# Kernel tuning notes

Measured on AMD Instinct MI355X. Metric: run time of the kernel, lower is better.

The kernel has to match this reference:

```python
import jax, jax.numpy as jnp
import numpy as np

B, N, SEQ, PRED = 32, 128, 336, 96
DIN, DEMB, HID, G, K = 16, 32, 64, 8, 25
END = DEMB + 2  # 2 decomposition channels + dy embedding
T = SEQ + PRED


def setup_inputs() -> dict:
    key = jax.random.key(0)
    ks = jax.random.split(key, 22)
    s = 0.02
    p = lambda k, shape: jax.random.normal(k, shape, dtype=jnp.float32) * s
    return {
        "x": jax.random.normal(ks[0], (B, N, SEQ), dtype=jnp.float32),
        "dy": jax.random.normal(ks[1], (B, N, T, DIN), dtype=jnp.float32),
        "gi": jax.random.randint(ks[2], (N,), 0, G),
        "dy_w": p(ks[3], (DEMB, DIN)), "dy_b": p(ks[4], (DEMB,)),
        "w_seas": p(ks[5], (G, PRED, SEQ)), "b_seas": p(ks[6], (G, PRED)),
        "w_trend": p(ks[7], (G, PRED, SEQ)), "b_trend": p(ks[8], (G, PRED)),
        "w_res": p(ks[9], (G, PRED, SEQ)), "b_res": p(ks[10], (G, PRED)),
        "w1_end": p(ks[11], (G, HID, END)), "b1_end": p(ks[12], (G, HID)),
        "w2_end": p(ks[13], (G, 1, HID)), "b2_end": p(ks[14], (G, 1)),
        "w_ih": p(ks[15], (3 * HID, END)), "w_hh": p(ks[16], (3 * HID, HID)),
        "b_ih": p(ks[17], (3 * HID,)), "b_hh": p(ks[18], (3 * HID,)),
        "w_ap": p(ks[19], (1, HID)), "b_ap": p(ks[20], (1,)),
    }


def _moving_avg(x, k):
    # x: [b, seq, n]; edge-padded moving average over time (Autoformer series_decomp)
    pad = (k - 1) // 2
    xp = jnp.pad(x, ((0, 0), (pad, pad), (0, 0)), mode="edge")
    cs = jnp.cumsum(xp, axis=1)
    cs = jnp.concatenate([jnp.zeros_like(cs[:, :1]), cs], axis=1)
    return (cs[:, k:] - cs[:, :-k]) / k


def _gru(xseq, w_ih, w_hh, b_ih, b_hh):
    # torch nn.GRU, batch_first, gate order (r, z, n)
    h0 = jnp.zeros((xseq.shape[0], w_hh.shape[1]), dtype=xseq.dtype)
    gx = jnp.einsum("bti,gi->btg", xseq, w_ih) + b_ih  # input-side gates, precomputed
    def step(h, gxt):
        gh = h @ w_hh.T + b_hh
        ir, iz, inn = jnp.split(gxt, 3, axis=-1)
        hr, hz, hn = jnp.split(gh, 3, axis=-1)
        r = jax.nn.sigmoid(ir + hr)
        z = jax.nn.sigmoid(iz + hz)
        ng = jnp.tanh(inn + r * hn)
        h = (1.0 - z) * ng + z * h
        return h, h
    _, ys = jax.lax.scan(step, h0, gx.transpose(1, 0, 2))
    return ys.transpose(1, 0, 2)  # [b, t, hid]


def reference(x, dy, gi, dy_w, dy_b, w_seas, b_seas, w_trend, b_trend,
              w_res, b_res, w1_end, b1_end, w2_end, b2_end,
              w_ih, w_hh, b_ih, b_hh, w_ap, b_ap):
    # global residual path: per-group mean over member nodes
    cnt = jax.ops.segment_sum(jnp.ones((N,), x.dtype), gi, num_segments=G)  # [G]
    gsum = jax.ops.segment_sum(x.transpose(1, 0, 2), gi, num_segments=G)  # [G,b,seq]
    g_in = gsum / cnt[:, None, None]
    g_out = jnp.einsum("gps,gbs->gbp", w_res, g_in) + b_res[:, None, :]

    # series decomposition (node independent -> done once for all nodes)
    xt = x.transpose(0, 2, 1)  # [b, seq, n]
    trend = _moving_avg(xt, K)
    seasonal = xt - trend
    seasonal_init = seasonal.transpose(0, 2, 1)  # [b, n, seq]
    trend_init = trend.transpose(0, 2, 1)

    # per-group Linear(seq->pred) heads, gathered per node (MoE-style dispatch)
    seas_out = jnp.einsum("bns,nps->bnp", seasonal_init, w_seas[gi]) + b_seas[gi][None]
    trend_out = jnp.einsum("bns,nps->bnp", trend_init, w_trend[gi]) + b_trend[gi][None]

    dy_emb = jax.nn.relu(jnp.einsum("bnti,ei->bnte", dy, dy_w) + dy_b)  # [b,n,T,DEMB]

    hidden_former = jnp.concatenate(
        [seasonal_init[..., None], trend_init[..., None], dy_emb[:, :, :SEQ]], axis=-1)
    hidden_after = jnp.concatenate(
        [seas_out[..., None], trend_out[..., None], dy_emb[:, :, SEQ:]], axis=-1)

    # per-group end MLP (Linear -> ReLU -> Linear), weights gathered per node
    w1g, b1g = w1_end[gi], b1_end[gi]
    w2g, b2g = w2_end[gi, 0], b2_end[gi, 0]
    def end_mlp(h):
        z = jax.nn.relu(jnp.einsum("bnte,nhe->bnth", h, w1g) + b1g[None, :, None, :])
        return jnp.einsum("bnth,nh->bnt", z, w2g) + b2g[None, :, None]

    out_former = end_mlp(hidden_former) + g_in[gi].transpose(1, 0, 2)
    out_after = end_mlp(hidden_after) + g_out[gi].transpose(1, 0, 2)

    att_f = _gru(hidden_former.mean(axis=1), w_ih, w_hh, b_ih, b_hh)
    att_a = _gru(hidden_after.mean(axis=1), w_ih, w_hh, b_ih, b_hh)
    atten_former = jax.nn.sigmoid(att_f @ w_ap.T + b_ap)[..., 0]
    atten_after = jax.nn.sigmoid(att_a @ w_ap.T + b_ap)[..., 0]
    return (out_former, atten_former, out_after, atten_after)
```

## Files before the change

### kernel.cpp

```cpp
#include <hip/hip_runtime.h>
#include <math.h>

#define BB 32
#define NN 128
#define SEQL 336
#define PREDL 96
#define DINC 16
#define DEMBC 32
#define HIDC 64
#define GG 8
#define KWIN 25
#define ENDC 34
#define TT 432

#define OFF_SEAS   0
#define OFF_TREND  (OFF_SEAS + BB*NN*SEQL)
#define OFF_GIN    (OFF_TREND + BB*NN*SEQL)
#define OFF_GOUT   (OFF_GIN + GG*BB*SEQL)
#define OFF_SEASO  (OFF_GOUT + GG*BB*PREDL)
#define OFF_TRENDO (OFF_SEASO + BB*NN*PREDL)
#define OFF_GX     (OFF_TRENDO + BB*NN*PREDL)
#define OFF_HIST   (OFF_GX + BB*TT*192)

#define OUT_FORMER 0
#define OUT_ATTF   (BB*NN*SEQL)
#define OUT_AFTER  (OUT_ATTF + BB*SEQL)
#define OUT_ATTA   (OUT_AFTER + BB*NN*PREDL)

__device__ __forceinline__ float fsig(float x) { return 1.0f/(1.0f + __expf(-x)); }
__device__ __forceinline__ float ftanh(float x) { return 1.0f - 2.0f/(__expf(2.0f*x) + 1.0f); }

__global__ __launch_bounds__(384) void k_group_mean(const float* __restrict__ x,
                                                    const int* __restrict__ gi,
                                                    float* __restrict__ g_in) {
    int g = blockIdx.x, b = blockIdx.y;
    __shared__ int sgi[NN];
    __shared__ float scnt;
    int tid = threadIdx.x;
    if (tid < NN) sgi[tid] = gi[tid];
    __syncthreads();
    if (tid == 0) {
        int c = 0;
        for (int n = 0; n < NN; n++) if (sgi[n] == g) c++;
        scnt = (float)c;
    }
    __syncthreads();
    float inv = 1.0f / scnt;
    for (int s = tid; s < SEQL; s += 384) {
        float sum = 0.0f;
        for (int n = 0; n < NN; n++)
            if (sgi[n] == g) sum += x[(b*NN + n)*SEQL + s];
        g_in[(g*BB + b)*SEQL + s] = sum * inv;
    }
}

__global__ void k_gout(const float* __restrict__ g_in, const float* __restrict__ w_res,
                       const float* __restrict__ b_res, float* __restrict__ g_out) {
    int idx = blockIdx.x*blockDim.x + threadIdx.x;
    if (idx >= GG*BB*PREDL) return;
    int p = idx % PREDL;
    int b = (idx / PREDL) % BB;
    int g = idx / (PREDL*BB);
    const float* gr = g_in + (g*BB + b)*SEQL;
    const float* wr = w_res + (g*PREDL + p)*SEQL;
    float acc = b_res[g*PREDL + p];
    for (int s = 0; s < SEQL; s++) acc += gr[s]*wr[s];
    g_out[idx] = acc;
}

__global__ void k_decomp(const float* __restrict__ x, float* __restrict__ seasonal,
                         float* __restrict__ trend) {
    int idx = blockIdx.x*blockDim.x + threadIdx.x;
    if (idx >= BB*NN*SEQL) return;
    int t = idx % SEQL;
    int bn = idx / SEQL;
    const float* xr = x + bn*SEQL;
    float s = 0.0f;
    #pragma unroll
    for (int d = -12; d <= 12; d++) {
        int j = t + d;
        j = j < 0 ? 0 : (j >= SEQL ? SEQL-1 : j);
        s += xr[j];
    }
    float tr = s * (1.0f/KWIN);
    trend[idx] = tr;
    seasonal[idx] = xr[t] - tr;
}

__global__ __launch_bounds__(128) void k_heads(const float* __restrict__ seasonal,
                                               const float* __restrict__ trend,
                                               const int* __restrict__ gi,
                                               const float* __restrict__ w_seas,
                                               const float* __restrict__ b_seas,
                                               const float* __restrict__ w_trend,
                                               const float* __restrict__ b_trend,
                                               float* __restrict__ seas_out,
                                               float* __restrict__ trend_out) {
    int bn = blockIdx.x;
    int n = bn % NN;
    int g = gi[n];
    __shared__ float ss[SEQL];
    __shared__ float st[SEQL];
    for (int s = threadIdx.x; s < SEQL/4; s += 128) {
        ((float4*)ss)[s] = ((const float4*)(seasonal + bn*SEQL))[s];
        ((float4*)st)[s] = ((const float4*)(trend + bn*SEQL))[s];
    }
    __syncthreads();
    int p = threadIdx.x;
    if (p < PREDL) {
        const float4* wsr = (const float4*)(w_seas + (g*PREDL + p)*SEQL);
        const float4* wtr = (const float4*)(w_trend + (g*PREDL + p)*SEQL);
        float a = b_seas[g*PREDL + p];
        float c = b_trend[g*PREDL + p];
        #pragma unroll 4
        for (int s4 = 0; s4 < SEQL/4; s4++) {
            float4 w0 = wsr[s4], w1 = wtr[s4];
            float4 d0 = ((const float4*)ss)[s4], d1 = ((const float4*)st)[s4];
            a += w0.x*d0.x + w0.y*d0.y + w0.z*d0.z + w0.w*d0.w;
            c += w1.x*d1.x + w1.y*d1.y + w1.z*d1.z + w1.w*d1.w;
        }
        seas_out[bn*PREDL + p] = a;
        trend_out[bn*PREDL + p] = c;
    }
}

__global__ __launch_bounds__(64) void k_hmean_gx(
    const float* __restrict__ seasonal, const float* __restrict__ trend,
    const float* __restrict__ seas_out, const float* __restrict__ trend_out,
    const float* __restrict__ dy, const float* __restrict__ dy_w,
    const float* __restrict__ dy_b, const float* __restrict__ w_ih,
    const float* __restrict__ b_ih, const float* __restrict__ b_hh,
    float* __restrict__ gx)
{
    int bt = blockIdx.x;
    int b = bt / TT, t = bt % TT;
    int lane = threadIdx.x;
    float v[ENDC];
    #pragma unroll
    for (int e = 0; e < ENDC; e++) v[e] = 0.0f;
    #pragma unroll
    for (int q = 0; q < 2; q++) {
        int n = lane + q*64;
        int bn = b*NN + n;
        if (t < SEQL) {
            v[0] += seasonal[bn*SEQL + t];
            v[1] += trend[bn*SEQL + t];
        } else {
            int p = t - SEQL;
            v[0] += seas_out[bn*PREDL + p];
            v[1] += trend_out[bn*PREDL + p];
        }
        const float4* dyr = (const float4*)(dy + ((size_t)bn*TT + t)*DINC);
        float4 d0 = dyr[0], d1 = dyr[1], d2 = dyr[2], d3 = dyr[3];
        float dv[DINC] = {d0.x,d0.y,d0.z,d0.w, d1.x,d1.y,d1.z,d1.w,
                          d2.x,d2.y,d2.z,d2.w, d3.x,d3.y,d3.z,d3.w};
        #pragma unroll 4
        for (int e = 0; e < DEMBC; e++) {
            float a = dy_b[e];
            #pragma unroll
            for (int i = 0; i < DINC; i++) a = fmaf(dv[i], dy_w[e*DINC + i], a);
            v[2+e] += fmaxf(a, 0.0f);
        }
    }
    #pragma unroll
    for (int e = 0; e < ENDC; e++) {
        float s = v[e];
        s += __shfl_xor(s, 32, 64);
        s += __shfl_xor(s, 16, 64);
        s += __shfl_xor(s, 8, 64);
        s += __shfl_xor(s, 4, 64);
        s += __shfl_xor(s, 2, 64);
        s += __shfl_xor(s, 1, 64);
        v[e] = s * (1.0f/NN);
    }
    #pragma unroll
    for (int gate = 0; gate < 3; gate++) {
        int j = gate*64 + lane;
        const float* w = w_ih + j*ENDC;
        float a = b_ih[j] + (gate < 2 ? b_hh[j] : 0.0f);
        #pragma unroll
        for (int e = 0; e < ENDC; e++) a = fmaf(v[e], w[e], a);
        gx[(size_t)bt*192 + j] = a;
    }
}

__global__ __launch_bounds__(512, 2) void k_mlp_gru(
    const float* __restrict__ seasonal, const float* __restrict__ trend,
    const float* __restrict__ seas_out, const float* __restrict__ trend_out,
    const float* __restrict__ g_in, const float* __restrict__ g_out,
    const int* __restrict__ gi, const float* __restrict__ dy,
    const float* __restrict__ dy_w, const float* __restrict__ dy_b,
    const float* __restrict__ w1_end, const float* __restrict__ b1_end,
    const float* __restrict__ w2_end, const float* __restrict__ b2_end,
    const float* __restrict__ gx, const float* __restrict__ w_hh,
    const float* __restrict__ b_hh, const float* __restrict__ w_ap,
    const float* __restrict__ b_ap, float* __restrict__ hist,
    float* __restrict__ out)
{
    __shared__ float hs[2*HIDC];
    int tid = threadIdx.x;

    if (blockIdx.x < 64) {
        if (tid >= 64) return;
        int lane = tid;
        int blk = blockIdx.x;
        int b = blk & 31;
        bool former = (blk < 32);
        int steps = former ? SEQL : PREDL;
        int t0 = former ? 0 : SEQL;
        float* hb = hist + (former ? (size_t)b*SEQL*HIDC
                                   : (size_t)BB*SEQL*HIDC + (size_t)b*PREDL*HIDC);
        float wr_[HIDC], wz_[HIDC], wn_[HIDC];
        #pragma unroll
        for (int k = 0; k < HIDC; k++) wr_[k] = w_hh[lane*HIDC + k];
        #pragma unroll
        for (int k = 0; k < HIDC; k++) wz_[k] = w_hh[(lane+64)*HIDC + k];
        #pragma unroll
        for (int k = 0; k < HIDC; k++) wn_[k] = w_hh[(lane+128)*HIDC + k];
        float bhn = b_hh[lane + 128];
        hs[lane] = 0.0f;
        float h = 0.0f;
        const float* gxb = gx + (size_t)(b*TT + t0)*192;
        float c_r = gxb[lane], c_z = gxb[64+lane], c_n = gxb[128+lane];
        float n_r = 0.f, n_z = 0.f, n_n = 0.f;
        if (steps > 1) { n_r = gxb[192+lane]; n_z = gxb[256+lane]; n_n = gxb[320+lane]; }
        for (int s = 0; s < steps; s++) {
            float p_r = 0.f, p_z = 0.f, p_n = 0.f;
            if (s + 2 < steps) {
                const float* gp = gxb + (size_t)(s+2)*192;
                p_r = gp[lane]; p_z = gp[64+lane]; p_n = gp[128+lane];
            }
            const float* hh = hs + (s & 1)*HIDC;
            float ar = 0.f, az = 0.f, an = 0.f;
            #pragma unroll
            for (int k = 0; k < HIDC; k += 4) {
                float4 h4 = *(const float4*)&hh[k];
                ar = fmaf(h4.x, wr_[k],   ar); az = fmaf(h4.x, wz_[k],   az); an = fmaf(h4.x, wn_[k],   an);
                ar = fmaf(h4.y, wr_[k+1], ar); az = fmaf(h4.y, wz_[k+1], az); an = fmaf(h4.y, wn_[k+1], an);
                ar = fmaf(h4.z, wr_[k+2], ar); az = fmaf(h4.z, wz_[k+2], az); an = fmaf(h4.z, wn_[k+2], an);
                ar = fmaf(h4.w, wr_[k+3], ar); az = fmaf(h4.w, wz_[k+3], az); an = fmaf(h4.w, wn_[k+3], an);
            }
            float r = fsig(c_r + ar);
            float z = fsig(c_z + az);
            float tg = ftanh(c_n + r*(bhn + an));
            h = (1.0f - z)*tg + z*h;
            hs[((s+1) & 1)*HIDC + lane] = h;
            hb[(size_t)s*HIDC + lane] = h;
            c_r = n_r; c_z = n_z; c_n = n_n;
            n_r = p_r; n_z = p_z; n_n = p_n;
        }
        float bap = b_ap[0];
        float* attn = out + (former ? (OUT_ATTF + b*SEQL) : (OUT_ATTA + b*PREDL));
        for (int t = lane; t < steps; t += 64) {
            const float* hr = hb + (size_t)t*HIDC;
            float a = 0.f;
            #pragma unroll 16
            for (int k = 0; k < HIDC; k++) a = fmaf(hr[k], w_ap[k], a);
            attn[t] = fsig(a + bap);
        }
        return;
    }

    int bn = blockIdx.x - 64;
    int b = bn / NN, n = bn % NN;
    int g = gi[n];
    int t = tid;
    if (t >= TT) return;

    const float4* dyr = (const float4*)(dy + ((size_t)bn*TT + t)*DINC);
    float4 d0 = dyr[0], d1 = dyr[1], d2 = dyr[2], d3 = dyr[3];
    float dv[DINC] = {d0.x,d0.y,d0.z,d0.w, d1.x,d1.y,d1.z,d1.w,
                      d2.x,d2.y,d2.z,d2.w, d3.x,d3.y,d3.z,d3.w};
    float hv[36];
    #pragma unroll 4
    for (int e = 0; e < DEMBC; e++) {
        float a = dy_b[e];
        #pragma unroll
        for (int i = 0; i < DINC; i++) a = fmaf(dv[i], dy_w[e*DINC + i], a);
        hv[2+e] = fmaxf(a, 0.0f);
    }
    float addv;
    if (t < SEQL) {
        hv[0] = seasonal[bn*SEQL + t];
        hv[1] = trend[bn*SEQL + t];
        addv = g_in[(g*BB + b)*SEQL + t];
    } else {
        int p = t - SEQL;
        hv[0] = seas_out[bn*PREDL + p];
        hv[1] = trend_out[bn*PREDL + p];
        addv = g_out[(g*BB + b)*PREDL + p];
    }
    float acc = b2_end[g];
    const float* w1g = w1_end + g*HIDC*ENDC;
    const float* b1g = b1_end + g*HIDC;
    const float* w2g = w2_end + g*HIDC;
    #pragma unroll 4
    for (int hq = 0; hq < HIDC; hq++) {
        const float* wrow = w1g + hq*ENDC;
        float a = b1g[hq];
        #pragma unroll
        for (int e = 0; e < ENDC; e++) a = fmaf(hv[e], wrow[e], a);
        acc = fmaf(fmaxf(a, 0.0f), w2g[hq], acc);
    }
    acc += addv;
    if (t < SEQL) out[OUT_FORMER + bn*SEQL + t] = acc;
    else          out[OUT_AFTER + bn*PREDL + (t - SEQL)] = acc;
}

extern "C" void kernel_launch(void* const* d_in, const int* in_sizes, int n_in,
                              void* d_out, int out_size, void* d_ws, size_t ws_size,
                              hipStream_t stream) {
    (void)in_sizes; (void)n_in; (void)out_size; (void)ws_size;
    const float* x       = (const float*)d_in[0];
    const float* dy      = (const float*)d_in[1];
    const int*   gi      = (const int*)  d_in[2];
    const float* dy_w    = (const float*)d_in[3];
    const float* dy_b    = (const float*)d_in[4];
    const float* w_seas  = (const float*)d_in[5];
    const float* b_seas  = (const float*)d_in[6];
    const float* w_trend = (const float*)d_in[7];
    const float* b_trend = (const float*)d_in[8];
    const float* w_res   = (const float*)d_in[9];
    const float* b_res   = (const float*)d_in[10];
    const float* w1_end  = (const float*)d_in[11];
    const float* b1_end  = (const float*)d_in[12];
    const float* w2_end  = (const float*)d_in[13];
    const float* b2_end  = (const float*)d_in[14];
    const float* w_ih    = (const float*)d_in[15];
    const float* w_hh    = (const float*)d_in[16];
    const float* b_ih    = (const float*)d_in[17];
    const float* b_hh    = (const float*)d_in[18];
    const float* w_ap    = (const float*)d_in[19];
    const float* b_ap    = (const float*)d_in[20];
    float* ws  = (float*)d_ws;
    float* out = (float*)d_out;

    hipLaunchKernelGGL(k_group_mean, dim3(GG, BB), dim3(384), 0, stream, x, gi, ws + OFF_GIN);
    hipLaunchKernelGGL(k_decomp, dim3((BB*NN*SEQL + 255)/256), dim3(256), 0, stream,
                       x, ws + OFF_SEAS, ws + OFF_TREND);
    hipLaunchKernelGGL(k_gout, dim3((GG*BB*PREDL + 255)/256), dim3(256), 0, stream,
                       ws + OFF_GIN, w_res, b_res, ws + OFF_GOUT);
    hipLaunchKernelGGL(k_heads, dim3(BB*NN), dim3(128), 0, stream,
                       ws + OFF_SEAS, ws + OFF_TREND, gi, w_seas, b_seas, w_trend, b_trend,
                       ws + OFF_SEASO, ws + OFF_TRENDO);
    hipLaunchKernelGGL(k_hmean_gx, dim3(BB*TT), dim3(64), 0, stream,
                       ws + OFF_SEAS, ws + OFF_TREND, ws + OFF_SEASO, ws + OFF_TRENDO,
                       dy, dy_w, dy_b, w_ih, b_ih, b_hh, ws + OFF_GX);
    hipLaunchKernelGGL(k_mlp_gru, dim3(64 + BB*NN), dim3(512), 0, stream,
                       ws + OFF_SEAS, ws + OFF_TREND, ws + OFF_SEASO, ws + OFF_TRENDO,
                       ws + OFF_GIN, ws + OFF_GOUT, gi, dy, dy_w, dy_b,
                       w1_end, b1_end, w2_end, b2_end,
                       ws + OFF_GX, w_hh, b_hh, w_ap, b_ap, ws + OFF_HIST, out);
}
```

Measured before the change: 848.8 us.

## Fuse dy-mean gate projection into end-MLP kernel and split GRU out

Merges the group-mean and residual-head kernels into one, with the group mean kept in shared memory for the head's dot products. The separate per-(b,t) mean and input-gate kernel is folded into a tiled end-MLP kernel: each block covers 64 timesteps for one batch, sums the hidden features across nodes in registers and shared memory, and then computes the gx projection. This reads dy once instead of twice and removes two launches. In exchange, the GRU recurrence now runs as its own kernel after the MLP instead of overlapping with it. The MLP grid also shrinks to 224 large blocks, each looping over 16 nodes per wave.

```diff
diff --git a/kernel.cpp b/kernel.cpp
--- a/kernel.cpp
+++ b/kernel.cpp
@@ -30,11 +30,15 @@
 __device__ __forceinline__ float fsig(float x) { return 1.0f/(1.0f + __expf(-x)); }
 __device__ __forceinline__ float ftanh(float x) { return 1.0f - 2.0f/(__expf(2.0f*x) + 1.0f); }
 
-__global__ __launch_bounds__(384) void k_group_mean(const float* __restrict__ x,
-                                                    const int* __restrict__ gi,
-                                                    float* __restrict__ g_in) {
+__global__ __launch_bounds__(384) void k_gm_gout(const float* __restrict__ x,
+                                                 const int* __restrict__ gi,
+                                                 const float* __restrict__ w_res,
+                                                 const float* __restrict__ b_res,
+                                                 float* __restrict__ g_in,
+                                                 float* __restrict__ g_out) {
     int g = blockIdx.x, b = blockIdx.y;
     __shared__ int sgi[NN];
+    __shared__ float sg[SEQL];
     __shared__ float scnt;
     int tid = threadIdx.x;
     if (tid < NN) sgi[tid] = gi[tid];
@@ -50,22 +54,23 @@
         float sum = 0.0f;
         for (int n = 0; n < NN; n++)
             if (sgi[n] == g) sum += x[(b*NN + n)*SEQL + s];
-        g_in[(g*BB + b)*SEQL + s] = sum * inv;
-    }
-}
-
-__global__ void k_gout(const float* __restrict__ g_in, const float* __restrict__ w_res,
-                       const float* __restrict__ b_res, float* __restrict__ g_out) {
-    int idx = blockIdx.x*blockDim.x + threadIdx.x;
-    if (idx >= GG*BB*PREDL) return;
-    int p = idx % PREDL;
-    int b = (idx / PREDL) % BB;
-    int g = idx / (PREDL*BB);
-    const float* gr = g_in + (g*BB + b)*SEQL;
-    const float* wr = w_res + (g*PREDL + p)*SEQL;
-    float acc = b_res[g*PREDL + p];
-    for (int s = 0; s < SEQL; s++) acc += gr[s]*wr[s];
-    g_out[idx] = acc;
+        float v = sum * inv;
+        sg[s] = v;
+        g_in[(g*BB + b)*SEQL + s] = v;
+    }
+    __syncthreads();
+    int p = tid;
+    if (p < PREDL) {
+        const float4* wr = (const float4*)(w_res + (g*PREDL + p)*SEQL);
+        float acc = b_res[g*PREDL + p];
+        #pragma unroll 4
+        for (int s4 = 0; s4 < SEQL/4; s4++) {
+            float4 w = wr[s4];
+            float4 d = ((const float4*)sg)[s4];
+            acc += w.x*d.x + w.y*d.y + w.z*d.z + w.w*d.w;
+        }
+        g_out[(g*BB + b)*PREDL + p] = acc;
+    }
 }
 
 __global__ void k_decomp(const float* __restrict__ x, float* __restrict__ seasonal,
@@ -124,67 +129,7 @@
     }
 }
 
-__global__ __launch_bounds__(64) void k_hmean_gx(
-    const float* __restrict__ seasonal, const float* __restrict__ trend,
-    const float* __restrict__ seas_out, const float* __restrict__ trend_out,
-    const float* __restrict__ dy, const float* __restrict__ dy_w,
-    const float* __restrict__ dy_b, const float* __restrict__ w_ih,
-    const float* __restrict__ b_ih, const float* __restrict__ b_hh,
-    float* __restrict__ gx)
-{
-    int bt = blockIdx.x;
-    int b = bt / TT, t = bt % TT;
-    int lane = threadIdx.x;
-    float v[ENDC];
-    #pragma unroll
-    for (int e = 0; e < ENDC; e++) v[e] = 0.0f;
-    #pragma unroll
-    for (int q = 0; q < 2; q++) {
-        int n = lane + q*64;
-        int bn = b*NN + n;
-        if (t < SEQL) {
-            v[0] += seasonal[bn*SEQL + t];
-            v[1] += trend[bn*SEQL + t];
-        } else {
-            int p = t - SEQL;
-            v[0] += seas_out[bn*PREDL + p];
-            v[1] += trend_out[bn*PREDL + p];
-        }
-        const float4* dyr = (const float4*)(dy + ((size_t)bn*TT + t)*DINC);
-        float4 d0 = dyr[0], d1 = dyr[1], d2 = dyr[2], d3 = dyr[3];
-        float dv[DINC] = {d0.x,d0.y,d0.z,d0.w, d1.x,d1.y,d1.z,d1.w,
-                          d2.x,d2.y,d2.z,d2.w, d3.x,d3.y,d3.z,d3.w};
-        #pragma unroll 4
-        for (int e = 0; e < DEMBC; e++) {
-            float a = dy_b[e];
-            #pragma unroll
-            for (int i = 0; i < DINC; i++) a = fmaf(dv[i], dy_w[e*DINC + i], a);
-            v[2+e] += fmaxf(a, 0.0f);
-        }
-    }
-    #pragma unroll
-    for (int e = 0; e < ENDC; e++) {
-        float s = v[e];
-        s += __shfl_xor(s, 32, 64);
-        s += __shfl_xor(s, 16, 64);
-        s += __shfl_xor(s, 8, 64);
-        s += __shfl_xor(s, 4, 64);
-        s += __shfl_xor(s, 2, 64);
-        s += __shfl_xor(s, 1, 64);
-        v[e] = s * (1.0f/NN);
-    }
-    #pragma unroll
-    for (int gate = 0; gate < 3; gate++) {
-        int j = gate*64 + lane;
-        const float* w = w_ih + j*ENDC;
-        float a = b_ih[j] + (gate < 2 ? b_hh[j] : 0.0f);
-        #pragma unroll
-        for (int e = 0; e < ENDC; e++) a = fmaf(v[e], w[e], a);
-        gx[(size_t)bt*192 + j] = a;
-    }
-}
-
-__global__ __launch_bounds__(512, 2) void k_mlp_gru(
+__global__ __launch_bounds__(512, 1) void k_mlp_all(
     const float* __restrict__ seasonal, const float* __restrict__ trend,
     const float* __restrict__ seas_out, const float* __restrict__ trend_out,
     const float* __restrict__ g_in, const float* __restrict__ g_out,
@@ -192,119 +137,167 @@
     const float* __restrict__ dy_w, const float* __restrict__ dy_b,
     const float* __restrict__ w1_end, const float* __restrict__ b1_end,
     const float* __restrict__ w2_end, const float* __restrict__ b2_end,
+    const float* __restrict__ w_ih, const float* __restrict__ b_ih,
+    const float* __restrict__ b_hh, float* __restrict__ gx,
+    float* __restrict__ out)
+{
+    __shared__ float s_wih[192][35];
+    __shared__ float s_hsum[64][35];
+    int tile = blockIdx.x;
+    int b = blockIdx.y;
+    int tid = threadIdx.x;
+    int lane = tid & 63, wave = tid >> 6;
+    int t = tile*64 + lane;
+    bool tvalid = (t < TT);
+    int tc = tvalid ? t : (TT-1);
+
+    for (int i = tid; i < 192*ENDC; i += 512) s_wih[i/ENDC][i%ENDC] = w_ih[i];
+    for (int i = tid; i < 64*35; i += 512) (&s_hsum[0][0])[i] = 0.0f;
+    __syncthreads();
+
+    float hsum[ENDC];
+    #pragma unroll
+    for (int e = 0; e < ENDC; e++) hsum[e] = 0.0f;
+
+    int wbase = __builtin_amdgcn_readfirstlane(wave);
+
+    for (int ni = 0; ni < 16; ni++) {
+        int n = wbase + ni*8;
+        int bn = b*NN + n;
+        int g = gi[n];
+        const float4* dyr = (const float4*)(dy + ((size_t)bn*TT + tc)*DINC);
+        float4 d0 = dyr[0], d1 = dyr[1], d2 = dyr[2], d3 = dyr[3];
+        float dv[DINC] = {d0.x,d0.y,d0.z,d0.w, d1.x,d1.y,d1.z,d1.w,
+                          d2.x,d2.y,d2.z,d2.w, d3.x,d3.y,d3.z,d3.w};
+        float hv[ENDC];
+        #pragma unroll 4
+        for (int e = 0; e < DEMBC; e++) {
+            float a = dy_b[e];
+            #pragma unroll
+            for (int i = 0; i < DINC; i++) a = fmaf(dv[i], dy_w[e*DINC + i], a);
+            hv[2+e] = fmaxf(a, 0.0f);
+        }
+        float addv;
+        if (tc < SEQL) {
+            hv[0] = seasonal[bn*SEQL + tc];
+            hv[1] = trend[bn*SEQL + tc];
+            addv = g_in[(g*BB + b)*SEQL + tc];
+        } else {
+            int p = tc - SEQL;
+            hv[0] = seas_out[bn*PREDL + p];
+            hv[1] = trend_out[bn*PREDL + p];
+            addv = g_out[(g*BB + b)*PREDL + p];
+        }
+        float acc = b2_end[g];
+        const float* w1g = w1_end + g*HIDC*ENDC;
+        const float* b1g = b1_end + g*HIDC;
+        const float* w2g = w2_end + g*HIDC;
+        #pragma unroll 4
+        for (int hq = 0; hq < HIDC; hq++) {
+            const float* wrow = w1g + hq*ENDC;
+            float a = b1g[hq];
+            #pragma unroll
+            for (int e = 0; e < ENDC; e++) a = fmaf(hv[e], wrow[e], a);
+            acc = fmaf(fmaxf(a, 0.0f), w2g[hq], acc);
+        }
+        acc += addv;
+        if (tvalid) {
+            if (t < SEQL) out[OUT_FORMER + bn*SEQL + t] = acc;
+            else          out[OUT_AFTER + bn*PREDL + (t - SEQL)] = acc;
+        }
+        #pragma unroll
+        for (int e = 0; e < ENDC; e++) hsum[e] += hv[e];
+    }
+
+    for (int w = 0; w < 8; w++) {
+        if (wave == w) {
+            #pragma unroll
+            for (int e = 0; e < ENDC; e++) s_hsum[lane][e] += hsum[e];
+        }
+        __syncthreads();
+    }
+    for (int i = tid; i < 64*ENDC; i += 512) {
+        int tt2 = i / ENDC, e = i % ENDC;
+        s_hsum[tt2][e] *= (1.0f/NN);
+    }
+    __syncthreads();
+
+    for (int it = 0; it < 24; it++) {
+        int idx = tid + it*512;
+        int j = idx % 192, tt2 = idx / 192;
+        int tg = tile*64 + tt2;
+        if (tg < TT) {
+            float a = b_ih[j] + (j < 2*HIDC ? b_hh[j] : 0.0f);
+            #pragma unroll
+            for (int e = 0; e < ENDC; e++) a = fmaf(s_hsum[tt2][e], s_wih[j][e], a);
+            gx[((size_t)b*TT + tg)*192 + j] = a;
+        }
+    }
+}
+
+__global__ __launch_bounds__(64, 1) void k_gru(
     const float* __restrict__ gx, const float* __restrict__ w_hh,
     const float* __restrict__ b_hh, const float* __restrict__ w_ap,
     const float* __restrict__ b_ap, float* __restrict__ hist,
     float* __restrict__ out)
 {
     __shared__ float hs[2*HIDC];
-    int tid = threadIdx.x;
-
-    if (blockIdx.x < 64) {
-        if (tid >= 64) return;
-        int lane = tid;
-        int blk = blockIdx.x;
-        int b = blk & 31;
-        bool former = (blk < 32);
-        int steps = former ? SEQL : PREDL;
-        int t0 = former ? 0 : SEQL;
-        float* hb = hist + (former ? (size_t)b*SEQL*HIDC
-                                   : (size_t)BB*SEQL*HIDC + (size_t)b*PREDL*HIDC);
-        float wr_[HIDC], wz_[HIDC], wn_[HIDC];
+    int lane = threadIdx.x;
+    int blk = blockIdx.x;
+    int b = blk & 31;
+    bool former = (blk < 32);
+    int steps = former ? SEQL : PREDL;
+    int t0 = former ? 0 : SEQL;
+    float* hb = hist + (former ? (size_t)b*SEQL*HIDC
+                               : (size_t)BB*SEQL*HIDC + (size_t)b*PREDL*HIDC);
+    float wr_[HIDC], wz_[HIDC], wn_[HIDC];
+    #pragma unroll
+    for (int k = 0; k < HIDC; k++) wr_[k] = w_hh[lane*HIDC + k];
+    #pragma unroll
+    for (int k = 0; k < HIDC; k++) wz_[k] = w_hh[(lane+64)*HIDC + k];
+    #pragma unroll
+    for (int k = 0; k < HIDC; k++) wn_[k] = w_hh[(lane+128)*HIDC + k];
+    float bhn = b_hh[lane + 128];
+    hs[lane] = 0.0f;
+    float h = 0.0f;
+    const float* gxb = gx + (size_t)(b*TT + t0)*192;
+    float c_r = gxb[lane], c_z = gxb[64+lane], c_n = gxb[128+lane];
+    float n_r = 0.f, n_z = 0.f, n_n = 0.f;
+    if (steps > 1) { n_r = gxb[192+lane]; n_z = gxb[256+lane]; n_n = gxb[320+lane]; }
+    for (int s = 0; s < steps; s++) {
+        float p_r = 0.f, p_z = 0.f, p_n = 0.f;
+        if (s + 2 < steps) {
+            const float* gp = gxb + (size_t)(s+2)*192;
+            p_r = gp[lane]; p_z = gp[64+lane]; p_n = gp[128+lane];
+        }
+        const float* hh = hs + (s & 1)*HIDC;
+        float ar = 0.f, az = 0.f, an = 0.f;
         #pragma unroll
-        for (int k = 0; k < HIDC; k++) wr_[k] = w_hh[lane*HIDC + k];
-        #pragma unroll
-        for (int k = 0; k < HIDC; k++) wz_[k] = w_hh[(lane+64)*HIDC + k];
-        #pragma unroll
-        for (int k = 0; k < HIDC; k++) wn_[k] = w_hh[(lane+128)*HIDC + k];
-        float bhn = b_hh[lane + 128];
-        hs[lane] = 0.0f;
-        float h = 0.0f;
-        const float* gxb = gx + (size_t)(b*TT + t0)*192;
-        float c_r = gxb[lane], c_z = gxb[64+lane], c_n = gxb[128+lane];
-        float n_r = 0.f, n_z = 0.f, n_n = 0.f;
-        if (steps > 1) { n_r = gxb[192+lane]; n_z = gxb[256+lane]; n_n = gxb[320+lane]; }
-        for (int s = 0; s < steps; s++) {
-            float p_r = 0.f, p_z = 0.f, p_n = 0.f;
-            if (s + 2 < steps) {
-                const float* gp = gxb + (size_t)(s+2)*192;
-                p_r = gp[lane]; p_z = gp[64+lane]; p_n = gp[128+lane];
-            }
-            const float* hh = hs + (s & 1)*HIDC;
-            float ar = 0.f, az = 0.f, an = 0.f;
-            #pragma unroll
-            for (int k = 0; k < HIDC; k += 4) {
-                float4 h4 = *(const float4*)&hh[k];
-                ar = fmaf(h4.x, wr_[k],   ar); az = fmaf(h4.x, wz_[k],   az); an = fmaf(h4.x, wn_[k],   an);
-                ar = fmaf(h4.y, wr_[k+1], ar); az = fmaf(h4.y, wz_[k+1], az); an = fmaf(h4.y, wn_[k+1], an);
-                ar = fmaf(h4.z, wr_[k+2], ar); az = fmaf(h4.z, wz_[k+2], az); an = fmaf(h4.z, wn_[k+2], an);
-                ar = fmaf(h4.w, wr_[k+3], ar); az = fmaf(h4.w, wz_[k+3], az); an = fmaf(h4.w, wn_[k+3], an);
-            }
-            float r = fsig(c_r + ar);
-            float z = fsig(c_z + az);
-            float tg = ftanh(c_n + r*(bhn + an));
-            h = (1.0f - z)*tg + z*h;
-            hs[((s+1) & 1)*HIDC + lane] = h;
-            hb[(size_t)s*HIDC + lane] = h;
-            c_r = n_r; c_z = n_z; c_n = n_n;
-            n_r = p_r; n_z = p_z; n_n = p_n;
-        }
-        float bap = b_ap[0];
-        float* attn = out + (former ? (OUT_ATTF + b*SEQL) : (OUT_ATTA + b*PREDL));
-        for (int t = lane; t < steps; t += 64) {
-            const float* hr = hb + (size_t)t*HIDC;
-            float a = 0.f;
-            #pragma unroll 16
-            for (int k = 0; k < HIDC; k++) a = fmaf(hr[k], w_ap[k], a);
-            attn[t] = fsig(a + bap);
-        }
-        return;
-    }
-
-    int bn = blockIdx.x - 64;
-    int b = bn / NN, n = bn % NN;
-    int g = gi[n];
-    int t = tid;
-    if (t >= TT) return;
-
-    const float4* dyr = (const float4*)(dy + ((size_t)bn*TT + t)*DINC);
-    float4 d0 = dyr[0], d1 = dyr[1], d2 = dyr[2], d3 = dyr[3];
-    float dv[DINC] = {d0.x,d0.y,d0.z,d0.w, d1.x,d1.y,d1.z,d1.w,
-                      d2.x,d2.y,d2.z,d2.w, d3.x,d3.y,d3.z,d3.w};
-    float hv[36];
-    #pragma unroll 4
-    for (int e = 0; e < DEMBC; e++) {
-        float a = dy_b[e];
-        #pragma unroll
-        for (int i = 0; i < DINC; i++) a = fmaf(dv[i], dy_w[e*DINC + i], a);
-        hv[2+e] = fmaxf(a, 0.0f);
-    }
-    float addv;
-    if (t < SEQL) {
-        hv[0] = seasonal[bn*SEQL + t];
-        hv[1] = trend[bn*SEQL + t];
-        addv = g_in[(g*BB + b)*SEQL + t];
-    } else {
-        int p = t - SEQL;
-        hv[0] = seas_out[bn*PREDL + p];
-        hv[1] = trend_out[bn*PREDL + p];
-        addv = g_out[(g*BB + b)*PREDL + p];
-    }
-    float acc = b2_end[g];
-    const float* w1g = w1_end + g*HIDC*ENDC;
-    const float* b1g = b1_end + g*HIDC;
-    const float* w2g = w2_end + g*HIDC;
-    #pragma unroll 4
-    for (int hq = 0; hq < HIDC; hq++) {
-        const float* wrow = w1g + hq*ENDC;
-        float a = b1g[hq];
-        #pragma unroll
-        for (int e = 0; e < ENDC; e++) a = fmaf(hv[e], wrow[e], a);
-        acc = fmaf(fmaxf(a, 0.0f), w2g[hq], acc);
-    }
-    acc += addv;
-    if (t < SEQL) out[OUT_FORMER + bn*SEQL + t] = acc;
-    else          out[OUT_AFTER + bn*PREDL + (t - SEQL)] = acc;
+        for (int k = 0; k < HIDC; k += 4) {
+            float4 h4 = *(const float4*)&hh[k];
+            ar = fmaf(h4.x, wr_[k],   ar); az = fmaf(h4.x, wz_[k],   az); an = fmaf(h4.x, wn_[k],   an);
+            ar = fmaf(h4.y, wr_[k+1], ar); az = fmaf(h4.y, wz_[k+1], az); an = fmaf(h4.y, wn_[k+1], an);
+            ar = fmaf(h4.z, wr_[k+2], ar); az = fmaf(h4.z, wz_[k+2], az); an = fmaf(h4.z, wn_[k+2], an);
+            ar = fmaf(h4.w, wr_[k+3], ar); az = fmaf(h4.w, wz_[k+3], az); an = fmaf(h4.w, wn_[k+3], an);
+        }
+        float r = fsig(c_r + ar);
+        float z = fsig(c_z + az);
+        float tg = ftanh(c_n + r*(bhn + an));
+        h = (1.0f - z)*tg + z*h;
+        hs[((s+1) & 1)*HIDC + lane] = h;
+        hb[(size_t)s*HIDC + lane] = h;
+        c_r = n_r; c_z = n_z; c_n = n_n;
+        n_r = p_r; n_z = p_z; n_n = p_n;
+    }
+    float bap = b_ap[0];
+    float* attn = out + (former ? (OUT_ATTF + b*SEQL) : (OUT_ATTA + b*PREDL));
+    for (int t = lane; t < steps; t += 64) {
+        const float* hr = hb + (size_t)t*HIDC;
+        float a = 0.f;
+        #pragma unroll 16
+        for (int k = 0; k < HIDC; k++) a = fmaf(hr[k], w_ap[k], a);
+        attn[t] = fsig(a + bap);
+    }
 }
 
 extern "C" void kernel_launch(void* const* d_in, const int* in_sizes, int n_in,
@@ -335,20 +328,18 @@
     float* ws  = (float*)d_ws;
     float* out = (float*)d_out;
 
-    hipLaunchKernelGGL(k_group_mean, dim3(GG, BB), dim3(384), 0, stream, x, gi, ws + OFF_GIN);
+    hipLaunchKernelGGL(k_gm_gout, dim3(GG, BB), dim3(384), 0, stream,
+                       x, gi, w_res, b_res, ws + OFF_GIN, ws + OFF_GOUT);
     hipLaunchKernelGGL(k_decomp, dim3((BB*NN*SEQL + 255)/256), dim3(256), 0, stream,
                        x, ws + OFF_SEAS, ws + OFF_TREND);
-    hipLaunchKernelGGL(k_gout, dim3((GG*BB*PREDL + 255)/256), dim3(256), 0, stream,
-                       ws + OFF_GIN, w_res, b_res, ws + OFF_GOUT);
     hipLaunchKernelGGL(k_heads, dim3(BB*NN), dim3(128), 0, stream,
                        ws + OFF_SEAS, ws + OFF_TREND, gi, w_seas, b_seas, w_trend, b_trend,
                        ws + OFF_SEASO, ws + OFF_TRENDO);
-    hipLaunchKernelGGL(k_hmean_gx, dim3(BB*TT), dim3(64), 0, stream,
-                       ws + OFF_SEAS, ws + OFF_TREND, ws + OFF_SEASO, ws + OFF_TRENDO,
-                       dy, dy_w, dy_b, w_ih, b_ih, b_hh, ws + OFF_GX);
-    hipLaunchKernelGGL(k_mlp_gru, dim3(64 + BB*NN), dim3(512), 0, stream,
+    hipLaunchKernelGGL(k_mlp_all, dim3(7, 32), dim3(512), 0, stream,
                        ws + OFF_SEAS, ws + OFF_TREND, ws + OFF_SEASO, ws + OFF_TRENDO,
                        ws + OFF_GIN, ws + OFF_GOUT, gi, dy, dy_w, dy_b,
                        w1_end, b1_end, w2_end, b2_end,
+                       w_ih, b_ih, b_hh, ws + OFF_GX, out);
+    hipLaunchKernelGGL(k_gru, dim3(64), dim3(64), 0, stream,
                        ws + OFF_GX, w_hh, b_hh, w_ap, b_ap, ws + OFF_HIST, out);
 }
```

Result: no change. 857.6 us (+1.0%).
